# Optimization experiments

Hardware: AMD Instinct MI355X
Metric: run time of the kernel (lower is better)

Reference implementation:

```python
import jax, jax.numpy as jnp
import numpy as np

B, N, IN_DIM, D, H = 8, 1024, 128, 32, 8  # batch, nodes, in_dim, out_dim(per head), heads


def setup_inputs() -> dict:
    key = jax.random.key(0)
    ks = jax.random.split(key, 10)
    s = 1.0 / np.sqrt(IN_DIM)
    return {
        "h": jax.random.normal(ks[0], (B, N, IN_DIM), jnp.float32),
        "A": jax.random.randint(ks[1], (B, N, N), 0, 6, jnp.int32),  # hop distances
        "lengths": jax.random.randint(ks[2], (B,), 1, N + 1, jnp.int32),
        "alpha": jax.random.uniform(ks[3], (1,), jnp.float32, 0.1, 0.9),
        "Wq": jax.random.normal(ks[4], (H * D, IN_DIM), jnp.float32) * s,
        "bq": jax.random.normal(ks[5], (H * D,), jnp.float32) * 0.01,
        "Wk": jax.random.normal(ks[6], (H * D, IN_DIM), jnp.float32) * s,
        "bk": jax.random.normal(ks[7], (H * D,), jnp.float32) * 0.01,
        "Wv": jax.random.normal(ks[8], (H * D, IN_DIM), jnp.float32) * s,
        "bv": jax.random.normal(ks[9], (H * D,), jnp.float32) * 0.01,
    }


def reference(h, A, lengths, alpha, Wq, bq, Wk, bk, Wv, bv):
    b, n, _ = h.shape

    def proj(W, bvec):
        # [b, n, H*D] -> [b, H, n, D]
        return (h @ W.T + bvec).reshape(b, n, H, D).transpose(0, 2, 1, 3)

    Q, K, V = proj(Wq, bq), proj(Wk, bk), proj(Wv, bv)

    att = jnp.einsum("bhnd,bhmd->bhnm", Q, K)  # [b, H, n, n]
    pad = jnp.arange(n)[None, :] >= lengths[:, None]  # [b, n], True = padded node
    att = jnp.where(pad[:, None, None, :], -jnp.inf, att)  # mask key axis
    att = jax.nn.softmax(att / jnp.sqrt(jnp.asarray(D, att.dtype)), axis=-1)
    att = jnp.where(pad[:, None, :, None], jnp.asarray(0, att.dtype), att)  # zero padded query rows

    m1 = (A == 1)
    m2 = (A > 1)

    def masked_mean(a, m):
        mf = m[:, None, :, :].astype(a.dtype)
        cnt = H * jnp.sum(m)
        return jnp.sum(a * mf) / cnt.astype(a.dtype)

    pre_d1 = masked_mean(att, m1)
    pre_d2 = masked_mean(att, m2)

    # phi: adjacency-aware reweighting, att * alpha**A (hop-distance decay)
    att = att * jnp.power(alpha[0], A.astype(att.dtype))[:, None, :, :]

    post_d1 = masked_mean(att, m1)
    post_d2 = masked_mean(att, m2)

    h_heads = jnp.einsum("bhnm,bhmd->bhnd", att, V)  # [b, H, n, D]
    return h_heads, pre_d1, pre_d2, post_d1, post_d2
```

## Files before the change

kernel.cpp:

```cpp
#include <hip/hip_runtime.h>
#include <math.h>

#define BB 8
#define NN 1024
#define IND 128
#define DD 32
#define HH 8
#define KT 64
#define QT 64


__global__ __launch_bounds__(256) void proj_kernel(
    const float* __restrict__ h,
    const float* __restrict__ Wq, const float* __restrict__ bq,
    const float* __restrict__ Wk, const float* __restrict__ bk,
    const float* __restrict__ Wv, const float* __restrict__ bv,
    const int* __restrict__ lengths,
    float* __restrict__ Q, float* __restrict__ K, float* __restrict__ V)
{
    const int cb = blockIdx.x;
    const int rb = blockIdx.y;
    if (((rb & 15) * 64) >= lengths[rb >> 4]) return;

    const int t  = threadIdx.x;
    __shared__ float Xs[64][IND + 1];
    __shared__ float Ws[64][IND + 1];

    const int which = cb >> 2;
    const int c0    = (cb & 3) * 64;
    const float* Wsrc = (which == 0) ? Wq : (which == 1) ? Wk : Wv;
    const float* bsrc = (which == 0) ? bq : (which == 1) ? bk : bv;
    float* Out        = (which == 0) ? Q  : (which == 1) ? K  : V;

    #pragma unroll
    for (int i = 0; i < 8; ++i) {
        int e = (i * 256 + t) * 4;
        int r = e >> 7;
        int c = e & 127;
        float4 x = *(const float4*)(&h[(size_t)(rb * 64 + r) * IND + c]);
        Xs[r][c] = x.x; Xs[r][c + 1] = x.y; Xs[r][c + 2] = x.z; Xs[r][c + 3] = x.w;
        float4 w = *(const float4*)(&Wsrc[(size_t)(c0 + r) * IND + c]);
        Ws[r][c] = w.x; Ws[r][c + 1] = w.y; Ws[r][c + 2] = w.z; Ws[r][c + 3] = w.w;
    }
    __syncthreads();

    const int tr = (t >> 4) * 4;
    const int tc = (t & 15) * 4;
    float acc[4][4] = {};
    #pragma unroll 4
    for (int k = 0; k < IND; ++k) {
        float a0 = Xs[tr + 0][k], a1 = Xs[tr + 1][k], a2 = Xs[tr + 2][k], a3 = Xs[tr + 3][k];
        float w0 = Ws[tc + 0][k], w1 = Ws[tc + 1][k], w2 = Ws[tc + 2][k], w3 = Ws[tc + 3][k];
        acc[0][0] = fmaf(a0, w0, acc[0][0]); acc[0][1] = fmaf(a0, w1, acc[0][1]);
        acc[0][2] = fmaf(a0, w2, acc[0][2]); acc[0][3] = fmaf(a0, w3, acc[0][3]);
        acc[1][0] = fmaf(a1, w0, acc[1][0]); acc[1][1] = fmaf(a1, w1, acc[1][1]);
        acc[1][2] = fmaf(a1, w2, acc[1][2]); acc[1][3] = fmaf(a1, w3, acc[1][3]);
        acc[2][0] = fmaf(a2, w0, acc[2][0]); acc[2][1] = fmaf(a2, w1, acc[2][1]);
        acc[2][2] = fmaf(a2, w2, acc[2][2]); acc[2][3] = fmaf(a2, w3, acc[2][3]);
        acc[3][0] = fmaf(a3, w0, acc[3][0]); acc[3][1] = fmaf(a3, w1, acc[3][1]);
        acc[3][2] = fmaf(a3, w2, acc[3][2]); acc[3][3] = fmaf(a3, w3, acc[3][3]);
    }

    #pragma unroll
    for (int i = 0; i < 4; ++i) {
        int r = rb * 64 + tr + i;
        int bb = r >> 10, n = r & 1023;
        #pragma unroll
        for (int j = 0; j < 4; ++j) {
            int o = tc + j + c0;
            int hh = o >> 5, dd = o & 31;
            Out[(((size_t)bb * HH + hh) * NN + n) * DD + dd] = acc[i][j] + bsrc[o];
        }
    }
}

__global__ __launch_bounds__(256) void pack_kernel(
    const int* __restrict__ A, unsigned char* __restrict__ A8,
    unsigned long long* __restrict__ cnt)
{
    const int NT = (BB * NN * NN) / 4;
    unsigned c1 = 0, c2 = 0;
    for (int idx = blockIdx.x * 256 + threadIdx.x; idx < NT; idx += gridDim.x * 256) {
        int4 a = *(const int4*)&A[(size_t)idx * 4];
        unsigned packed = (unsigned)(a.x & 0xff) | ((unsigned)(a.y & 0xff) << 8) |
                          ((unsigned)(a.z & 0xff) << 16) | ((unsigned)(a.w & 0xff) << 24);
        *(unsigned*)&A8[(size_t)idx * 4] = packed;
        c1 += (a.x == 1) + (a.y == 1) + (a.z == 1) + (a.w == 1);
        c2 += (a.x > 1) + (a.y > 1) + (a.z > 1) + (a.w > 1);
    }
    #pragma unroll
    for (int off = 32; off; off >>= 1) {
        c1 += __shfl_down(c1, off);
        c2 += __shfl_down(c2, off);
    }
    __shared__ unsigned r1[4], r2[4];
    const int wave = threadIdx.x >> 6;
    if ((threadIdx.x & 63) == 0) { r1[wave] = c1; r2[wave] = c2; }
    __syncthreads();
    if (threadIdx.x == 0) {
        unsigned long long t1 = (unsigned long long)r1[0] + r1[1] + r1[2] + r1[3];
        unsigned long long t2 = (unsigned long long)r2[0] + r2[1] + r2[2] + r2[3];
        atomicAdd(&cnt[0], t1);
        atomicAdd(&cnt[32], t2);
    }
}

__global__ __launch_bounds__(256) void attn_kernel(
    const float* __restrict__ Q, const float* __restrict__ Kg, const float* __restrict__ Vg,
    const unsigned char* __restrict__ A8,
    const int* __restrict__ lengths, const float* __restrict__ alpha,
    float* __restrict__ out, double* __restrict__ sums)
{
    const int bid = blockIdx.x;
    const int qt = bid & 15;
    const int hh = (bid >> 4) & 7;
    const int b  = bid >> 7;
    const int t  = threadIdx.x;
    const int qg = t >> 3;
    const int lane8 = t & 7;

    const int len = lengths[b];
    const size_t base = ((size_t)b * HH + hh) * NN * DD;
    const int gq0 = qt * QT + qg;
    const int gq1 = gq0 + 32;

    if (qt * QT >= len) {
        float4 z = make_float4(0.f, 0.f, 0.f, 0.f);
        *(float4*)&out[base + (size_t)gq0 * DD + lane8 * 4] = z;
        *(float4*)&out[base + (size_t)gq1 * DD + lane8 * 4] = z;
        return;
    }

    __shared__ float Qs[QT][36];
    __shared__ float Ks[KT][36];
    __shared__ float Vs[KT][36];
    __shared__ unsigned char As[QT][80];
    __shared__ float red4[4][4];

    const float al  = alpha[0];
    const float l2a = __log2f(al);
    const float scale = 0.17677669529663687f;

    const int sr = t >> 3;
    const int sc = ((t & 7) - sr) & 7;

    #pragma unroll
    for (int i = 0; i < 2; ++i) {
        int r = i * 32 + sr;
        float4 v = *(const float4*)&Q[base + (size_t)(qt * QT + r) * DD + sc * 4];
        v.x *= scale; v.y *= scale; v.z *= scale; v.w *= scale;
        *(float4*)&Qs[r][sc * 4] = v;
    }

    float m0 = -1e30f, m1 = -1e30f, l0 = 0.f, l1 = 0.f;
    float acc0[32], acc1[32];
    #pragma unroll
    for (int d = 0; d < 32; ++d) { acc0[d] = 0.f; acc1[d] = 0.f; }
    float pr0_1 = 0.f, pr0_2 = 0.f, po0_1 = 0.f, po0_2 = 0.f;
    float pr1_1 = 0.f, pr1_2 = 0.f, po1_1 = 0.f, po1_2 = 0.f;

    for (int j0 = 0; j0 < len; j0 += KT) {
        __syncthreads();
        #pragma unroll
        for (int i = 0; i < 2; ++i) {
            int r = i * 32 + sr;
            *(float4*)&Ks[r][sc * 4] = *(const float4*)&Kg[base + (size_t)(j0 + r) * DD + sc * 4];
            *(float4*)&Vs[r][sc * 4] = *(const float4*)&Vg[base + (size_t)(j0 + r) * DD + sc * 4];
        }
        {
            int r = t >> 2, c = (t & 3) * 16;
            *(int4*)&As[r][c] = *(const int4*)&A8[((size_t)b * NN + qt * QT + r) * NN + j0 + c];
        }
        __syncthreads();

        float s0[8], s1[8];
        #pragma unroll
        for (int e = 0; e < 8; ++e) { s0[e] = 0.f; s1[e] = 0.f; }
        #pragma unroll
        for (int i = 0; i < 8; ++i) {
            float4 qa = *(const float4*)&Qs[qg][i * 4];
            float4 qb = *(const float4*)&Qs[qg + 32][i * 4];
            #pragma unroll
            for (int e = 0; e < 8; ++e) {
                float4 kv = *(const float4*)&Ks[e * 8 + lane8][i * 4];
                s0[e] = fmaf(qa.x, kv.x, s0[e]); s0[e] = fmaf(qa.y, kv.y, s0[e]);
                s0[e] = fmaf(qa.z, kv.z, s0[e]); s0[e] = fmaf(qa.w, kv.w, s0[e]);
                s1[e] = fmaf(qb.x, kv.x, s1[e]); s1[e] = fmaf(qb.y, kv.y, s1[e]);
                s1[e] = fmaf(qb.z, kv.z, s1[e]); s1[e] = fmaf(qb.w, kv.w, s1[e]);
            }
        }

        float tm0 = -INFINITY, tm1 = -INFINITY;
        #pragma unroll
        for (int e = 0; e < 8; ++e) {
            bool valid = (j0 + e * 8 + lane8) < len;
            s0[e] = valid ? s0[e] : -INFINITY;
            s1[e] = valid ? s1[e] : -INFINITY;
            tm0 = fmaxf(tm0, s0[e]); tm1 = fmaxf(tm1, s1[e]);
        }
        #pragma unroll
        for (int off = 1; off < 8; off <<= 1) {
            tm0 = fmaxf(tm0, __shfl_xor(tm0, off, 8));
            tm1 = fmaxf(tm1, __shfl_xor(tm1, off, 8));
        }
        if (tm0 > m0) {
            float scl = __expf(m0 - tm0);
            l0 *= scl; pr0_1 *= scl; pr0_2 *= scl; po0_1 *= scl; po0_2 *= scl;
            #pragma unroll
            for (int d = 0; d < 32; ++d) acc0[d] *= scl;
            m0 = tm0;
        }
        if (tm1 > m1) {
            float scl = __expf(m1 - tm1);
            l1 *= scl; pr1_1 *= scl; pr1_2 *= scl; po1_1 *= scl; po1_2 *= scl;
            #pragma unroll
            for (int d = 0; d < 32; ++d) acc1[d] *= scl;
            m1 = tm1;
        }

        #pragma unroll
        for (int e = 0; e < 8; ++e) {
            int j = e * 8 + lane8;
            float pe0 = __expf(s0[e] - m0);
            float pe1 = __expf(s1[e] - m1);
            l0 += pe0; l1 += pe1;
            int a0 = As[qg][j], a1 = As[qg + 32][j];
            float w0 = exp2f((float)a0 * l2a);
            float w1 = exp2f((float)a1 * l2a);
            float pw0 = pe0 * w0, pw1 = pe1 * w1;
            pr0_1 += (a0 == 1) ? pe0 : 0.f;  pr0_2 += (a0 > 1) ? pe0 : 0.f;
            po0_1 += (a0 == 1) ? pw0 : 0.f;  po0_2 += (a0 > 1) ? pw0 : 0.f;
            pr1_1 += (a1 == 1) ? pe1 : 0.f;  pr1_2 += (a1 > 1) ? pe1 : 0.f;
            po1_1 += (a1 == 1) ? pw1 : 0.f;  po1_2 += (a1 > 1) ? pw1 : 0.f;
            s0[e] = pw0; s1[e] = pw1;
        }

        #pragma unroll
        for (int e = 0; e < 8; ++e) {
            float pw0 = s0[e], pw1 = s1[e];
            #pragma unroll
            for (int i = 0; i < 8; ++i) {
                float4 vv = *(const float4*)&Vs[e * 8 + lane8][i * 4];
                acc0[i * 4 + 0] = fmaf(pw0, vv.x, acc0[i * 4 + 0]);
                acc0[i * 4 + 1] = fmaf(pw0, vv.y, acc0[i * 4 + 1]);
                acc0[i * 4 + 2] = fmaf(pw0, vv.z, acc0[i * 4 + 2]);
                acc0[i * 4 + 3] = fmaf(pw0, vv.w, acc0[i * 4 + 3]);
                acc1[i * 4 + 0] = fmaf(pw1, vv.x, acc1[i * 4 + 0]);
                acc1[i * 4 + 1] = fmaf(pw1, vv.y, acc1[i * 4 + 1]);
                acc1[i * 4 + 2] = fmaf(pw1, vv.z, acc1[i * 4 + 2]);
                acc1[i * 4 + 3] = fmaf(pw1, vv.w, acc1[i * 4 + 3]);
            }
        }
    }

    #pragma unroll
    for (int off = 1; off < 8; off <<= 1) {
        l0 += __shfl_xor(l0, off, 8);
        l1 += __shfl_xor(l1, off, 8);
    }
    const float inv0 = (gq0 < len) ? 1.f / l0 : 0.f;
    const float inv1 = (gq1 < len) ? 1.f / l1 : 0.f;

    #pragma unroll
    for (int off = 1; off < 8; off <<= 1) {
        #pragma unroll
        for (int d = 0; d < 32; ++d) {
            acc0[d] += __shfl_xor(acc0[d], off, 8);
            acc1[d] += __shfl_xor(acc1[d], off, 8);
        }
    }
    if (lane8 == 0) {
        #pragma unroll
        for (int i = 0; i < 8; ++i) {
            *(float4*)&out[base + (size_t)gq0 * DD + i * 4] =
                make_float4(acc0[i * 4 + 0] * inv0, acc0[i * 4 + 1] * inv0,
                            acc0[i * 4 + 2] * inv0, acc0[i * 4 + 3] * inv0);
            *(float4*)&out[base + (size_t)gq1 * DD + i * 4] =
                make_float4(acc1[i * 4 + 0] * inv1, acc1[i * 4 + 1] * inv1,
                            acc1[i * 4 + 2] * inv1, acc1[i * 4 + 3] * inv1);
        }
    }

    float v1 = pr0_1 * inv0 + pr1_1 * inv1;
    float v2 = pr0_2 * inv0 + pr1_2 * inv1;
    float v3 = po0_1 * inv0 + po1_1 * inv1;
    float v4 = po0_2 * inv0 + po1_2 * inv1;
    #pragma unroll
    for (int off = 1; off < 64; off <<= 1) {
        v1 += __shfl_xor(v1, off);
        v2 += __shfl_xor(v2, off);
        v3 += __shfl_xor(v3, off);
        v4 += __shfl_xor(v4, off);
    }
    const int wv = t >> 6;
    if ((t & 63) == 0) { red4[0][wv] = v1; red4[1][wv] = v2; red4[2][wv] = v3; red4[3][wv] = v4; }
    __syncthreads();
    if (t < 4) {
        float s = red4[t][0] + red4[t][1] + red4[t][2] + red4[t][3];
        atomicAdd(&sums[t * 32], (double)s);
    }
}

__global__ void fin_kernel(const double* __restrict__ sums,
                           const unsigned long long* __restrict__ cnt,
                           float* __restrict__ outtail)
{
    if (threadIdx.x == 0) {
        double c1 = (double)(cnt[0] * (unsigned long long)HH);
        double c2 = (double)(cnt[32] * (unsigned long long)HH);
        outtail[0] = (float)(sums[0]  / c1);
        outtail[1] = (float)(sums[32] / c2);
        outtail[2] = (float)(sums[64] / c1);
        outtail[3] = (float)(sums[96] / c2);
    }
}

extern "C" void kernel_launch(void* const* d_in, const int* in_sizes, int n_in,
                              void* d_out, int out_size, void* d_ws, size_t ws_size,
                              hipStream_t stream)
{
    const float* h   = (const float*)d_in[0];
    const int* A     = (const int*)d_in[1];
    const int* lens  = (const int*)d_in[2];
    const float* alp = (const float*)d_in[3];
    const float* Wq  = (const float*)d_in[4];
    const float* bq  = (const float*)d_in[5];
    const float* Wk  = (const float*)d_in[6];
    const float* bk  = (const float*)d_in[7];
    const float* Wv  = (const float*)d_in[8];
    const float* bv  = (const float*)d_in[9];

    float* outF = (float*)d_out;

    const size_t qkv = (size_t)BB * HH * NN * DD;
    float* Qw = (float*)d_ws;
    float* Kw = Qw + qkv;
    float* Vw = Kw + qkv;
    unsigned char* A8 = (unsigned char*)(Vw + qkv);
    double* sums = (double*)(A8 + (size_t)BB * NN * NN);
    unsigned long long* cnt = (unsigned long long*)(sums + 128);

    (void)hipMemsetAsync(sums, 0, 128 * sizeof(double) + 64 * sizeof(unsigned long long), stream);

    proj_kernel<<<dim3(12, 128), 256, 0, stream>>>(h, Wq, bq, Wk, bk, Wv, bv, lens, Qw, Kw, Vw);
    pack_kernel<<<1024, 256, 0, stream>>>(A, A8, cnt);
    attn_kernel<<<BB * HH * (NN / QT), 256, 0, stream>>>(Qw, Kw, Vw, A8, lens, alp, outF, sums);
    fin_kernel<<<1, 64, 0, stream>>>(sums, cnt, outF + qkv);
}
```

Before: 257.7 us.

## Split key tiles across two thread halves per block and merge softmax states

Attention blocks now use 512 threads where each 256-thread half processes alternating key tiles with its own K/V/A shared buffers. After the loop the halves merge their online-softmax max, sum, accumulators and masked-mean partials through shared memory. This shortens the serial key loop per block to reduce latency and load imbalance from long sequences, at the cost of more LDS per block, a merge step, and possible register pressure under the larger launch bound.

```diff
diff --git a/kernel.cpp b/kernel.cpp
--- a/kernel.cpp
+++ b/kernel.cpp
@@ -105,7 +105,7 @@
     }
 }
 
-__global__ __launch_bounds__(256) void attn_kernel(
+__global__ __launch_bounds__(512) void attn_kernel(
     const float* __restrict__ Q, const float* __restrict__ Kg, const float* __restrict__ Vg,
     const unsigned char* __restrict__ A8,
     const int* __restrict__ lengths, const float* __restrict__ alpha,
@@ -116,8 +116,10 @@
     const int hh = (bid >> 4) & 7;
     const int b  = bid >> 7;
     const int t  = threadIdx.x;
-    const int qg = t >> 3;
-    const int lane8 = t & 7;
+    const int half = t >> 8;
+    const int t2 = t & 255;
+    const int qg = t2 >> 3;
+    const int lane8 = t2 & 7;
 
     const int len = lengths[b];
     const size_t base = ((size_t)b * HH + hh) * NN * DD;
@@ -125,31 +127,37 @@
     const int gq1 = gq0 + 32;
 
     if (qt * QT >= len) {
-        float4 z = make_float4(0.f, 0.f, 0.f, 0.f);
-        *(float4*)&out[base + (size_t)gq0 * DD + lane8 * 4] = z;
-        *(float4*)&out[base + (size_t)gq1 * DD + lane8 * 4] = z;
+        if (t < 256) {
+            float4 z = make_float4(0.f, 0.f, 0.f, 0.f);
+            *(float4*)&out[base + (size_t)gq0 * DD + lane8 * 4] = z;
+            *(float4*)&out[base + (size_t)gq1 * DD + lane8 * 4] = z;
+        }
         return;
     }
 
-    __shared__ float Qs[QT][36];
-    __shared__ float Ks[KT][36];
-    __shared__ float Vs[KT][36];
-    __shared__ unsigned char As[QT][80];
-    __shared__ float red4[4][4];
+    __shared__ __align__(16) char smem[56448];
+    float (*Qs)[36]          = (float (*)[36])smem;
+    float (*Ks)[36]          = (float (*)[36])(smem + 9216 + half * 9216);
+    float (*Vs)[36]          = (float (*)[36])(smem + 27648 + half * 9216);
+    unsigned char (*Asl)[80] = (unsigned char (*)[80])(smem + 46080 + half * 5120);
+    float* mrg  = (float*)(smem + 46080);
+    float* redp = (float*)(smem + 56320);
 
     const float al  = alpha[0];
     const float l2a = __log2f(al);
     const float scale = 0.17677669529663687f;
 
-    const int sr = t >> 3;
-    const int sc = ((t & 7) - sr) & 7;
-
-    #pragma unroll
-    for (int i = 0; i < 2; ++i) {
-        int r = i * 32 + sr;
-        float4 v = *(const float4*)&Q[base + (size_t)(qt * QT + r) * DD + sc * 4];
-        v.x *= scale; v.y *= scale; v.z *= scale; v.w *= scale;
-        *(float4*)&Qs[r][sc * 4] = v;
+    const int sr = t2 >> 3;
+    const int sc = ((t2 & 7) - sr) & 7;
+
+    if (t < 256) {
+        #pragma unroll
+        for (int i = 0; i < 2; ++i) {
+            int r = i * 32 + sr;
+            float4 v = *(const float4*)&Q[base + (size_t)(qt * QT + r) * DD + sc * 4];
+            v.x *= scale; v.y *= scale; v.z *= scale; v.w *= scale;
+            *(float4*)&Qs[r][sc * 4] = v;
+        }
     }
 
     float m0 = -1e30f, m1 = -1e30f, l0 = 0.f, l1 = 0.f;
@@ -159,17 +167,22 @@
     float pr0_1 = 0.f, pr0_2 = 0.f, po0_1 = 0.f, po0_2 = 0.f;
     float pr1_1 = 0.f, pr1_2 = 0.f, po1_1 = 0.f, po1_2 = 0.f;
 
-    for (int j0 = 0; j0 < len; j0 += KT) {
+    const int ntiles = (len + KT - 1) / KT;
+    const int nit = (ntiles + 1) >> 1;
+
+    for (int it = 0; it < nit; ++it) {
+        const int j0  = (2 * it + half) * KT;
+        const int j0c = (j0 < len) ? j0 : 0;
         __syncthreads();
         #pragma unroll
         for (int i = 0; i < 2; ++i) {
             int r = i * 32 + sr;
-            *(float4*)&Ks[r][sc * 4] = *(const float4*)&Kg[base + (size_t)(j0 + r) * DD + sc * 4];
-            *(float4*)&Vs[r][sc * 4] = *(const float4*)&Vg[base + (size_t)(j0 + r) * DD + sc * 4];
+            *(float4*)&Ks[r][sc * 4] = *(const float4*)&Kg[base + (size_t)(j0c + r) * DD + sc * 4];
+            *(float4*)&Vs[r][sc * 4] = *(const float4*)&Vg[base + (size_t)(j0c + r) * DD + sc * 4];
         }
         {
-            int r = t >> 2, c = (t & 3) * 16;
-            *(int4*)&As[r][c] = *(const int4*)&A8[((size_t)b * NN + qt * QT + r) * NN + j0 + c];
+            int r = t2 >> 2, c = (t2 & 3) * 16;
+            *(int4*)&Asl[r][c] = *(const int4*)&A8[((size_t)b * NN + qt * QT + r) * NN + j0c + c];
         }
         __syncthreads();
 
@@ -224,7 +237,7 @@
             float pe0 = __expf(s0[e] - m0);
             float pe1 = __expf(s1[e] - m1);
             l0 += pe0; l1 += pe1;
-            int a0 = As[qg][j], a1 = As[qg + 32][j];
+            int a0 = Asl[qg][j], a1 = Asl[qg + 32][j];
             float w0 = exp2f((float)a0 * l2a);
             float w1 = exp2f((float)a1 * l2a);
             float pw0 = pe0 * w0, pw1 = pe1 * w1;
@@ -255,36 +268,76 @@
 
     #pragma unroll
     for (int off = 1; off < 8; off <<= 1) {
-        l0 += __shfl_xor(l0, off, 8);
-        l1 += __shfl_xor(l1, off, 8);
-    }
-    const float inv0 = (gq0 < len) ? 1.f / l0 : 0.f;
-    const float inv1 = (gq1 < len) ? 1.f / l1 : 0.f;
-
-    #pragma unroll
-    for (int off = 1; off < 8; off <<= 1) {
+        l0 += __shfl_xor(l0, off, 8);       l1 += __shfl_xor(l1, off, 8);
+        pr0_1 += __shfl_xor(pr0_1, off, 8); pr0_2 += __shfl_xor(pr0_2, off, 8);
+        po0_1 += __shfl_xor(po0_1, off, 8); po0_2 += __shfl_xor(po0_2, off, 8);
+        pr1_1 += __shfl_xor(pr1_1, off, 8); pr1_2 += __shfl_xor(pr1_2, off, 8);
+        po1_1 += __shfl_xor(po1_1, off, 8); po1_2 += __shfl_xor(po1_2, off, 8);
         #pragma unroll
         for (int d = 0; d < 32; ++d) {
             acc0[d] += __shfl_xor(acc0[d], off, 8);
             acc1[d] += __shfl_xor(acc1[d], off, 8);
         }
     }
-    if (lane8 == 0) {
-        #pragma unroll
-        for (int i = 0; i < 8; ++i) {
-            *(float4*)&out[base + (size_t)gq0 * DD + i * 4] =
-                make_float4(acc0[i * 4 + 0] * inv0, acc0[i * 4 + 1] * inv0,
-                            acc0[i * 4 + 2] * inv0, acc0[i * 4 + 3] * inv0);
-            *(float4*)&out[base + (size_t)gq1 * DD + i * 4] =
-                make_float4(acc1[i * 4 + 0] * inv1, acc1[i * 4 + 1] * inv1,
-                            acc1[i * 4 + 2] * inv1, acc1[i * 4 + 3] * inv1);
-        }
-    }
-
-    float v1 = pr0_1 * inv0 + pr1_1 * inv1;
-    float v2 = pr0_2 * inv0 + pr1_2 * inv1;
-    float v3 = po0_1 * inv0 + po1_1 * inv1;
-    float v4 = po0_2 * inv0 + po1_2 * inv1;
+
+    __syncthreads();
+    if (half == 1 && lane8 == 0) {
+        float* r = &mrg[(size_t)qg * 40];
+        r[0] = m0; r[1] = l0; r[2] = pr0_1; r[3] = pr0_2; r[4] = po0_1; r[5] = po0_2;
+        #pragma unroll
+        for (int d = 0; d < 32; ++d) r[6 + d] = acc0[d];
+        float* r2 = &mrg[(size_t)(qg + 32) * 40];
+        r2[0] = m1; r2[1] = l1; r2[2] = pr1_1; r2[3] = pr1_2; r2[4] = po1_1; r2[5] = po1_2;
+        #pragma unroll
+        for (int d = 0; d < 32; ++d) r2[6 + d] = acc1[d];
+    }
+    __syncthreads();
+
+    float v1 = 0.f, v2 = 0.f, v3 = 0.f, v4 = 0.f;
+    if (half == 0) {
+        const int dsl = lane8 * 4;
+        {
+            const float* r = &mrg[(size_t)qg * 40];
+            float mB = r[0], LB = r[1];
+            float ms = fmaxf(m0, mB);
+            float fA = __expf(m0 - ms), fB = __expf(mB - ms);
+            float L = l0 * fA + LB * fB;
+            float inv = (gq0 < len) ? 1.f / L : 0.f;
+            float4 o;
+            o.x = (acc0[dsl + 0] * fA + r[6 + dsl + 0] * fB) * inv;
+            o.y = (acc0[dsl + 1] * fA + r[6 + dsl + 1] * fB) * inv;
+            o.z = (acc0[dsl + 2] * fA + r[6 + dsl + 2] * fB) * inv;
+            o.w = (acc0[dsl + 3] * fA + r[6 + dsl + 3] * fB) * inv;
+            *(float4*)&out[base + (size_t)gq0 * DD + dsl] = o;
+            if (lane8 == 0) {
+                v1 += (pr0_1 * fA + r[2] * fB) * inv;
+                v2 += (pr0_2 * fA + r[3] * fB) * inv;
+                v3 += (po0_1 * fA + r[4] * fB) * inv;
+                v4 += (po0_2 * fA + r[5] * fB) * inv;
+            }
+        }
+        {
+            const float* r = &mrg[(size_t)(qg + 32) * 40];
+            float mB = r[0], LB = r[1];
+            float ms = fmaxf(m1, mB);
+            float fA = __expf(m1 - ms), fB = __expf(mB - ms);
+            float L = l1 * fA + LB * fB;
+            float inv = (gq1 < len) ? 1.f / L : 0.f;
+            float4 o;
+            o.x = (acc1[dsl + 0] * fA + r[6 + dsl + 0] * fB) * inv;
+            o.y = (acc1[dsl + 1] * fA + r[6 + dsl + 1] * fB) * inv;
+            o.z = (acc1[dsl + 2] * fA + r[6 + dsl + 2] * fB) * inv;
+            o.w = (acc1[dsl + 3] * fA + r[6 + dsl + 3] * fB) * inv;
+            *(float4*)&out[base + (size_t)gq1 * DD + dsl] = o;
+            if (lane8 == 0) {
+                v1 += (pr1_1 * fA + r[2] * fB) * inv;
+                v2 += (pr1_2 * fA + r[3] * fB) * inv;
+                v3 += (po1_1 * fA + r[4] * fB) * inv;
+                v4 += (po1_2 * fA + r[5] * fB) * inv;
+            }
+        }
+    }
+
     #pragma unroll
     for (int off = 1; off < 64; off <<= 1) {
         v1 += __shfl_xor(v1, off);
@@ -293,10 +346,16 @@
         v4 += __shfl_xor(v4, off);
     }
     const int wv = t >> 6;
-    if ((t & 63) == 0) { red4[0][wv] = v1; red4[1][wv] = v2; red4[2][wv] = v3; red4[3][wv] = v4; }
+    __syncthreads();
+    if ((t & 63) == 0) {
+        redp[0 * 8 + wv] = v1; redp[1 * 8 + wv] = v2;
+        redp[2 * 8 + wv] = v3; redp[3 * 8 + wv] = v4;
+    }
     __syncthreads();
     if (t < 4) {
-        float s = red4[t][0] + red4[t][1] + red4[t][2] + red4[t][3];
+        float s = 0.f;
+        #pragma unroll
+        for (int w = 0; w < 8; ++w) s += redp[t * 8 + w];
         atomicAdd(&sums[t * 32], (double)s);
     }
 }
@@ -344,6 +403,6 @@
 
     proj_kernel<<<dim3(12, 128), 256, 0, stream>>>(h, Wq, bq, Wk, bk, Wv, bv, lens, Qw, Kw, Vw);
     pack_kernel<<<1024, 256, 0, stream>>>(A, A8, cnt);
-    attn_kernel<<<BB * HH * (NN / QT), 256, 0, stream>>>(Qw, Kw, Vw, A8, lens, alp, outF, sums);
+    attn_kernel<<<BB * HH * (NN / QT), 512, 0, stream>>>(Qw, Kw, Vw, A8, lens, alp, outF, sums);
     fin_kernel<<<1, 64, 0, stream>>>(sums, cnt, outF + qkv);
 }
```

Measured after the change: 623.5 us. 142% more time.

## Split attention key range in two blocks and merge partial softmax results

Applied to the files above, without the earlier changes.

Adds a split-K flash-attention variant in which each query tile is processed by two blocks, each covering half of the key tiles. Partial max, denominator, mask statistics and accumulators go to a workspace buffer, and a separate merge kernel rescales and combines them, writes the output and accumulates the masked means. This doubles the grid to improve occupancy and load balance when sequence lengths vary. The cost is an extra kernel launch plus partial-result traffic, and the new path only runs when the workspace is large enough.

```diff
diff --git a/kernel.cpp b/kernel.cpp
--- a/kernel.cpp
+++ b/kernel.cpp
@@ -105,6 +105,7 @@
     }
 }
 
+
 __global__ __launch_bounds__(256) void attn_kernel(
     const float* __restrict__ Q, const float* __restrict__ Kg, const float* __restrict__ Vg,
     const unsigned char* __restrict__ A8,
@@ -301,6 +302,246 @@
     }
 }
 
+__global__ __launch_bounds__(256) void attn_split_kernel(
+    const float* __restrict__ Q, const float* __restrict__ Kg, const float* __restrict__ Vg,
+    const unsigned char* __restrict__ A8,
+    const int* __restrict__ lengths, const float* __restrict__ alpha,
+    float* __restrict__ part)
+{
+    const int bidAll = blockIdx.x;
+    const int split = bidAll >> 10;
+    const int bid = bidAll & 1023;
+    const int qt = bid & 15;
+    const int hh = (bid >> 4) & 7;
+    const int b  = bid >> 7;
+    const int t  = threadIdx.x;
+    const int qg = t >> 3;
+    const int lane8 = t & 7;
+
+    const int len = lengths[b];
+    const size_t base = ((size_t)b * HH + hh) * NN * DD;
+
+    if (qt * QT >= len) return;
+
+    __shared__ float Qs[QT][36];
+    __shared__ float Ks[KT][36];
+    __shared__ float Vs[KT][36];
+    __shared__ unsigned char As[QT][80];
+
+    const float al  = alpha[0];
+    const float l2a = __log2f(al);
+    const float scale = 0.17677669529663687f;
+
+    const int sr = t >> 3;
+    const int sc = ((t & 7) - sr) & 7;
+
+    #pragma unroll
+    for (int i = 0; i < 2; ++i) {
+        int r = i * 32 + sr;
+        float4 v = *(const float4*)&Q[base + (size_t)(qt * QT + r) * DD + sc * 4];
+        v.x *= scale; v.y *= scale; v.z *= scale; v.w *= scale;
+        *(float4*)&Qs[r][sc * 4] = v;
+    }
+
+    float m0 = -1e30f, m1 = -1e30f, l0 = 0.f, l1 = 0.f;
+    float acc0[32], acc1[32];
+    #pragma unroll
+    for (int d = 0; d < 32; ++d) { acc0[d] = 0.f; acc1[d] = 0.f; }
+    float pr0_1 = 0.f, pr0_2 = 0.f, po0_1 = 0.f, po0_2 = 0.f;
+    float pr1_1 = 0.f, pr1_2 = 0.f, po1_1 = 0.f, po1_2 = 0.f;
+
+    const int ntiles = (len + KT - 1) / KT;
+    const int htiles = (ntiles + 1) >> 1;
+    const int t0 = split * htiles;
+    const int t1 = (ntiles < t0 + htiles) ? ntiles : (t0 + htiles);
+
+    for (int tt = t0; tt < t1; ++tt) {
+        const int j0 = tt * KT;
+        __syncthreads();
+        #pragma unroll
+        for (int i = 0; i < 2; ++i) {
+            int r = i * 32 + sr;
+            *(float4*)&Ks[r][sc * 4] = *(const float4*)&Kg[base + (size_t)(j0 + r) * DD + sc * 4];
+            *(float4*)&Vs[r][sc * 4] = *(const float4*)&Vg[base + (size_t)(j0 + r) * DD + sc * 4];
+        }
+        {
+            int r = t >> 2, c = (t & 3) * 16;
+            *(int4*)&As[r][c] = *(const int4*)&A8[((size_t)b * NN + qt * QT + r) * NN + j0 + c];
+        }
+        __syncthreads();
+
+        float s0[8], s1[8];
+        #pragma unroll
+        for (int e = 0; e < 8; ++e) { s0[e] = 0.f; s1[e] = 0.f; }
+        #pragma unroll
+        for (int i = 0; i < 8; ++i) {
+            float4 qa = *(const float4*)&Qs[qg][i * 4];
+            float4 qb = *(const float4*)&Qs[qg + 32][i * 4];
+            #pragma unroll
+            for (int e = 0; e < 8; ++e) {
+                float4 kv = *(const float4*)&Ks[e * 8 + lane8][i * 4];
+                s0[e] = fmaf(qa.x, kv.x, s0[e]); s0[e] = fmaf(qa.y, kv.y, s0[e]);
+                s0[e] = fmaf(qa.z, kv.z, s0[e]); s0[e] = fmaf(qa.w, kv.w, s0[e]);
+                s1[e] = fmaf(qb.x, kv.x, s1[e]); s1[e] = fmaf(qb.y, kv.y, s1[e]);
+                s1[e] = fmaf(qb.z, kv.z, s1[e]); s1[e] = fmaf(qb.w, kv.w, s1[e]);
+            }
+        }
+
+        float tm0 = -INFINITY, tm1 = -INFINITY;
+        #pragma unroll
+        for (int e = 0; e < 8; ++e) {
+            bool valid = (j0 + e * 8 + lane8) < len;
+            s0[e] = valid ? s0[e] : -INFINITY;
+            s1[e] = valid ? s1[e] : -INFINITY;
+            tm0 = fmaxf(tm0, s0[e]); tm1 = fmaxf(tm1, s1[e]);
+        }
+        #pragma unroll
+        for (int off = 1; off < 8; off <<= 1) {
+            tm0 = fmaxf(tm0, __shfl_xor(tm0, off, 8));
+            tm1 = fmaxf(tm1, __shfl_xor(tm1, off, 8));
+        }
+        if (tm0 > m0) {
+            float scl = __expf(m0 - tm0);
+            l0 *= scl; pr0_1 *= scl; pr0_2 *= scl; po0_1 *= scl; po0_2 *= scl;
+            #pragma unroll
+            for (int d = 0; d < 32; ++d) acc0[d] *= scl;
+            m0 = tm0;
+        }
+        if (tm1 > m1) {
+            float scl = __expf(m1 - tm1);
+            l1 *= scl; pr1_1 *= scl; pr1_2 *= scl; po1_1 *= scl; po1_2 *= scl;
+            #pragma unroll
+            for (int d = 0; d < 32; ++d) acc1[d] *= scl;
+            m1 = tm1;
+        }
+
+        #pragma unroll
+        for (int e = 0; e < 8; ++e) {
+            int j = e * 8 + lane8;
+            float pe0 = __expf(s0[e] - m0);
+            float pe1 = __expf(s1[e] - m1);
+            l0 += pe0; l1 += pe1;
+            int a0 = As[qg][j], a1 = As[qg + 32][j];
+            float w0 = exp2f((float)a0 * l2a);
+            float w1 = exp2f((float)a1 * l2a);
+            float pw0 = pe0 * w0, pw1 = pe1 * w1;
+            pr0_1 += (a0 == 1) ? pe0 : 0.f;  pr0_2 += (a0 > 1) ? pe0 : 0.f;
+            po0_1 += (a0 == 1) ? pw0 : 0.f;  po0_2 += (a0 > 1) ? pw0 : 0.f;
+            pr1_1 += (a1 == 1) ? pe1 : 0.f;  pr1_2 += (a1 > 1) ? pe1 : 0.f;
+            po1_1 += (a1 == 1) ? pw1 : 0.f;  po1_2 += (a1 > 1) ? pw1 : 0.f;
+            s0[e] = pw0; s1[e] = pw1;
+        }
+
+        #pragma unroll
+        for (int e = 0; e < 8; ++e) {
+            float pw0 = s0[e], pw1 = s1[e];
+            #pragma unroll
+            for (int i = 0; i < 8; ++i) {
+                float4 vv = *(const float4*)&Vs[e * 8 + lane8][i * 4];
+                acc0[i * 4 + 0] = fmaf(pw0, vv.x, acc0[i * 4 + 0]);
+                acc0[i * 4 + 1] = fmaf(pw0, vv.y, acc0[i * 4 + 1]);
+                acc0[i * 4 + 2] = fmaf(pw0, vv.z, acc0[i * 4 + 2]);
+                acc0[i * 4 + 3] = fmaf(pw0, vv.w, acc0[i * 4 + 3]);
+                acc1[i * 4 + 0] = fmaf(pw1, vv.x, acc1[i * 4 + 0]);
+                acc1[i * 4 + 1] = fmaf(pw1, vv.y, acc1[i * 4 + 1]);
+                acc1[i * 4 + 2] = fmaf(pw1, vv.z, acc1[i * 4 + 2]);
+                acc1[i * 4 + 3] = fmaf(pw1, vv.w, acc1[i * 4 + 3]);
+            }
+        }
+    }
+
+    #pragma unroll
+    for (int off = 1; off < 8; off <<= 1) {
+        l0 += __shfl_xor(l0, off, 8);       l1 += __shfl_xor(l1, off, 8);
+        pr0_1 += __shfl_xor(pr0_1, off, 8); pr0_2 += __shfl_xor(pr0_2, off, 8);
+        po0_1 += __shfl_xor(po0_1, off, 8); po0_2 += __shfl_xor(po0_2, off, 8);
+        pr1_1 += __shfl_xor(pr1_1, off, 8); pr1_2 += __shfl_xor(pr1_2, off, 8);
+        po1_1 += __shfl_xor(po1_1, off, 8); po1_2 += __shfl_xor(po1_2, off, 8);
+        #pragma unroll
+        for (int d = 0; d < 32; ++d) {
+            acc0[d] += __shfl_xor(acc0[d], off, 8);
+            acc1[d] += __shfl_xor(acc1[d], off, 8);
+        }
+    }
+
+    const int dsl = lane8 * 4;
+    float* st0 = part + (((size_t)split * 1024 + bid) * 64 + qg) * 40;
+    float* st1 = st0 + 32 * 40;
+    if (lane8 == 0) {
+        st0[0] = m0; st0[1] = l0; st0[2] = pr0_1; st0[3] = pr0_2; st0[4] = po0_1; st0[5] = po0_2;
+        st1[0] = m1; st1[1] = l1; st1[2] = pr1_1; st1[3] = pr1_2; st1[4] = po1_1; st1[5] = po1_2;
+    }
+    *(float4*)&st0[8 + dsl] = make_float4(acc0[dsl], acc0[dsl + 1], acc0[dsl + 2], acc0[dsl + 3]);
+    *(float4*)&st1[8 + dsl] = make_float4(acc1[dsl], acc1[dsl + 1], acc1[dsl + 2], acc1[dsl + 3]);
+}
+
+__global__ __launch_bounds__(256) void merge_kernel(
+    const float* __restrict__ part, const int* __restrict__ lengths,
+    float* __restrict__ out, double* __restrict__ sums)
+{
+    const int bid = blockIdx.x;
+    const int qt = bid & 15;
+    const int hh = (bid >> 4) & 7;
+    const int b  = bid >> 7;
+    const int t  = threadIdx.x;
+    const int qg = t >> 3;
+    const int lane8 = t & 7;
+    const int dsl = lane8 * 4;
+    const int len = lengths[b];
+    const size_t base = ((size_t)b * HH + hh) * NN * DD;
+
+    if (qt * QT >= len) {
+        float4 z = make_float4(0.f, 0.f, 0.f, 0.f);
+        *(float4*)&out[base + (size_t)(qt * QT + qg) * DD + dsl] = z;
+        *(float4*)&out[base + (size_t)(qt * QT + qg + 32) * DD + dsl] = z;
+        return;
+    }
+
+    float v1 = 0.f, v2 = 0.f, v3 = 0.f, v4 = 0.f;
+    #pragma unroll
+    for (int rr = 0; rr < 2; ++rr) {
+        const int row = qg + rr * 32;
+        const int gq = qt * QT + row;
+        const float* sA = part + (((size_t)0 * 1024 + bid) * 64 + row) * 40;
+        const float* sB = part + (((size_t)1 * 1024 + bid) * 64 + row) * 40;
+        float mA = sA[0], lA = sA[1], mB = sB[0], lB = sB[1];
+        float ms = fmaxf(mA, mB);
+        float fA = __expf(mA - ms), fB = __expf(mB - ms);
+        float L = lA * fA + lB * fB;
+        float inv = (gq < len) ? 1.f / L : 0.f;
+        float4 aA = *(const float4*)&sA[8 + dsl];
+        float4 aB = *(const float4*)&sB[8 + dsl];
+        float4 o;
+        o.x = (aA.x * fA + aB.x * fB) * inv;
+        o.y = (aA.y * fA + aB.y * fB) * inv;
+        o.z = (aA.z * fA + aB.z * fB) * inv;
+        o.w = (aA.w * fA + aB.w * fB) * inv;
+        *(float4*)&out[base + (size_t)gq * DD + dsl] = o;
+        if (lane8 == 0) {
+            v1 += (sA[2] * fA + sB[2] * fB) * inv;
+            v2 += (sA[3] * fA + sB[3] * fB) * inv;
+            v3 += (sA[4] * fA + sB[4] * fB) * inv;
+            v4 += (sA[5] * fA + sB[5] * fB) * inv;
+        }
+    }
+
+    __shared__ float red4[4][4];
+    #pragma unroll
+    for (int off = 1; off < 64; off <<= 1) {
+        v1 += __shfl_xor(v1, off);
+        v2 += __shfl_xor(v2, off);
+        v3 += __shfl_xor(v3, off);
+        v4 += __shfl_xor(v4, off);
+    }
+    const int wv = t >> 6;
+    if ((t & 63) == 0) { red4[0][wv] = v1; red4[1][wv] = v2; red4[2][wv] = v3; red4[3][wv] = v4; }
+    __syncthreads();
+    if (t < 4) {
+        float s = red4[t][0] + red4[t][1] + red4[t][2] + red4[t][3];
+        atomicAdd(&sums[t * 32], (double)s);
+    }
+}
+
 __global__ void fin_kernel(const double* __restrict__ sums,
                            const unsigned long long* __restrict__ cnt,
                            float* __restrict__ outtail)
@@ -339,11 +580,19 @@
     unsigned char* A8 = (unsigned char*)(Vw + qkv);
     double* sums = (double*)(A8 + (size_t)BB * NN * NN);
     unsigned long long* cnt = (unsigned long long*)(sums + 128);
+    float* part = (float*)(cnt + 64);
+
+    const size_t need = (size_t)((char*)(part + (size_t)2048 * 64 * 40) - (char*)d_ws);
 
     (void)hipMemsetAsync(sums, 0, 128 * sizeof(double) + 64 * sizeof(unsigned long long), stream);
 
     proj_kernel<<<dim3(12, 128), 256, 0, stream>>>(h, Wq, bq, Wk, bk, Wv, bv, lens, Qw, Kw, Vw);
     pack_kernel<<<1024, 256, 0, stream>>>(A, A8, cnt);
-    attn_kernel<<<BB * HH * (NN / QT), 256, 0, stream>>>(Qw, Kw, Vw, A8, lens, alp, outF, sums);
+    if (ws_size >= need) {
+        attn_split_kernel<<<2048, 256, 0, stream>>>(Qw, Kw, Vw, A8, lens, alp, part);
+        merge_kernel<<<1024, 256, 0, stream>>>(part, lens, outF, sums);
+    } else {
+        attn_kernel<<<1024, 256, 0, stream>>>(Qw, Kw, Vw, A8, lens, alp, outF, sums);
+    }
     fin_kernel<<<1, 64, 0, stream>>>(sums, cnt, outF + qkv);
 }
```

Result: no change. 255.4 us (-0.9%).

## Split attention key range across two blocks, merge partial softmax states, vectorize projection

Applied to the files above, without the earlier changes.

The attention kernel now splits each query tile's key tiles between two blocks. Each block writes its partial max, sum, masked-mean statistics and accumulators to a workspace, and a new merge kernel combines them with log-sum-exp rescaling. The aim is more parallelism and better load balance across variable-length batches, at the cost of an extra launch and extra global memory traffic for the partial states. The projection kernel also switches to float4 shared-memory loads with a strided thread-to-output mapping, and the pack kernel grid is doubled.

```diff
diff --git a/kernel.cpp b/kernel.cpp
--- a/kernel.cpp
+++ b/kernel.cpp
@@ -23,8 +23,8 @@
     if (((rb & 15) * 64) >= lengths[rb >> 4]) return;
 
     const int t  = threadIdx.x;
-    __shared__ float Xs[64][IND + 1];
-    __shared__ float Ws[64][IND + 1];
+    __shared__ float Xs[64][132];
+    __shared__ float Ws[64][132];
 
     const int which = cb >> 2;
     const int c0    = (cb & 3) * 64;
@@ -37,37 +37,39 @@
         int e = (i * 256 + t) * 4;
         int r = e >> 7;
         int c = e & 127;
-        float4 x = *(const float4*)(&h[(size_t)(rb * 64 + r) * IND + c]);
-        Xs[r][c] = x.x; Xs[r][c + 1] = x.y; Xs[r][c + 2] = x.z; Xs[r][c + 3] = x.w;
-        float4 w = *(const float4*)(&Wsrc[(size_t)(c0 + r) * IND + c]);
-        Ws[r][c] = w.x; Ws[r][c + 1] = w.y; Ws[r][c + 2] = w.z; Ws[r][c + 3] = w.w;
+        *(float4*)&Xs[r][c] = *(const float4*)(&h[(size_t)(rb * 64 + r) * IND + c]);
+        *(float4*)&Ws[r][c] = *(const float4*)(&Wsrc[(size_t)(c0 + r) * IND + c]);
     }
     __syncthreads();
 
-    const int tr = (t >> 4) * 4;
-    const int tc = (t & 15) * 4;
+    const int tr = t >> 4;
+    const int tc = t & 15;
     float acc[4][4] = {};
-    #pragma unroll 4
-    for (int k = 0; k < IND; ++k) {
-        float a0 = Xs[tr + 0][k], a1 = Xs[tr + 1][k], a2 = Xs[tr + 2][k], a3 = Xs[tr + 3][k];
-        float w0 = Ws[tc + 0][k], w1 = Ws[tc + 1][k], w2 = Ws[tc + 2][k], w3 = Ws[tc + 3][k];
-        acc[0][0] = fmaf(a0, w0, acc[0][0]); acc[0][1] = fmaf(a0, w1, acc[0][1]);
-        acc[0][2] = fmaf(a0, w2, acc[0][2]); acc[0][3] = fmaf(a0, w3, acc[0][3]);
-        acc[1][0] = fmaf(a1, w0, acc[1][0]); acc[1][1] = fmaf(a1, w1, acc[1][1]);
-        acc[1][2] = fmaf(a1, w2, acc[1][2]); acc[1][3] = fmaf(a1, w3, acc[1][3]);
-        acc[2][0] = fmaf(a2, w0, acc[2][0]); acc[2][1] = fmaf(a2, w1, acc[2][1]);
-        acc[2][2] = fmaf(a2, w2, acc[2][2]); acc[2][3] = fmaf(a2, w3, acc[2][3]);
-        acc[3][0] = fmaf(a3, w0, acc[3][0]); acc[3][1] = fmaf(a3, w1, acc[3][1]);
-        acc[3][2] = fmaf(a3, w2, acc[3][2]); acc[3][3] = fmaf(a3, w3, acc[3][3]);
+    for (int k = 0; k < IND; k += 4) {
+        float4 xa[4], wb[4];
+        #pragma unroll
+        for (int i = 0; i < 4; ++i) xa[i] = *(const float4*)&Xs[tr + i * 16][k];
+        #pragma unroll
+        for (int j = 0; j < 4; ++j) wb[j] = *(const float4*)&Ws[tc + j * 16][k];
+        #pragma unroll
+        for (int i = 0; i < 4; ++i) {
+            #pragma unroll
+            for (int j = 0; j < 4; ++j) {
+                acc[i][j] = fmaf(xa[i].x, wb[j].x, acc[i][j]);
+                acc[i][j] = fmaf(xa[i].y, wb[j].y, acc[i][j]);
+                acc[i][j] = fmaf(xa[i].z, wb[j].z, acc[i][j]);
+                acc[i][j] = fmaf(xa[i].w, wb[j].w, acc[i][j]);
+            }
+        }
     }
 
     #pragma unroll
     for (int i = 0; i < 4; ++i) {
-        int r = rb * 64 + tr + i;
+        int r = rb * 64 + tr + i * 16;
         int bb = r >> 10, n = r & 1023;
         #pragma unroll
         for (int j = 0; j < 4; ++j) {
-            int o = tc + j + c0;
+            int o = tc + j * 16 + c0;
             int hh = o >> 5, dd = o & 31;
             Out[(((size_t)bb * HH + hh) * NN + n) * DD + dd] = acc[i][j] + bsrc[o];
         }
@@ -105,13 +107,15 @@
     }
 }
 
-__global__ __launch_bounds__(256) void attn_kernel(
+__global__ __launch_bounds__(256) void attn_split_kernel(
     const float* __restrict__ Q, const float* __restrict__ Kg, const float* __restrict__ Vg,
     const unsigned char* __restrict__ A8,
     const int* __restrict__ lengths, const float* __restrict__ alpha,
-    float* __restrict__ out, double* __restrict__ sums)
-{
-    const int bid = blockIdx.x;
+    float* __restrict__ part)
+{
+    const int bidAll = blockIdx.x;
+    const int split = bidAll >> 10;
+    const int bid = bidAll & 1023;
     const int qt = bid & 15;
     const int hh = (bid >> 4) & 7;
     const int b  = bid >> 7;
@@ -121,21 +125,13 @@
 
     const int len = lengths[b];
     const size_t base = ((size_t)b * HH + hh) * NN * DD;
-    const int gq0 = qt * QT + qg;
-    const int gq1 = gq0 + 32;
-
-    if (qt * QT >= len) {
-        float4 z = make_float4(0.f, 0.f, 0.f, 0.f);
-        *(float4*)&out[base + (size_t)gq0 * DD + lane8 * 4] = z;
-        *(float4*)&out[base + (size_t)gq1 * DD + lane8 * 4] = z;
-        return;
-    }
+
+    if (qt * QT >= len) return;
 
     __shared__ float Qs[QT][36];
     __shared__ float Ks[KT][36];
     __shared__ float Vs[KT][36];
     __shared__ unsigned char As[QT][80];
-    __shared__ float red4[4][4];
 
     const float al  = alpha[0];
     const float l2a = __log2f(al);
@@ -159,7 +155,13 @@
     float pr0_1 = 0.f, pr0_2 = 0.f, po0_1 = 0.f, po0_2 = 0.f;
     float pr1_1 = 0.f, pr1_2 = 0.f, po1_1 = 0.f, po1_2 = 0.f;
 
-    for (int j0 = 0; j0 < len; j0 += KT) {
+    const int ntiles = (len + KT - 1) / KT;
+    const int htiles = (ntiles + 1) >> 1;
+    const int t0 = split * htiles;
+    const int t1 = (ntiles < t0 + htiles) ? ntiles : (t0 + htiles);
+
+    for (int tt = t0; tt < t1; ++tt) {
+        const int j0 = tt * KT;
         __syncthreads();
         #pragma unroll
         for (int i = 0; i < 2; ++i) {
@@ -255,36 +257,80 @@
 
     #pragma unroll
     for (int off = 1; off < 8; off <<= 1) {
-        l0 += __shfl_xor(l0, off, 8);
-        l1 += __shfl_xor(l1, off, 8);
-    }
-    const float inv0 = (gq0 < len) ? 1.f / l0 : 0.f;
-    const float inv1 = (gq1 < len) ? 1.f / l1 : 0.f;
-
-    #pragma unroll
-    for (int off = 1; off < 8; off <<= 1) {
+        l0 += __shfl_xor(l0, off, 8);       l1 += __shfl_xor(l1, off, 8);
+        pr0_1 += __shfl_xor(pr0_1, off, 8); pr0_2 += __shfl_xor(pr0_2, off, 8);
+        po0_1 += __shfl_xor(po0_1, off, 8); po0_2 += __shfl_xor(po0_2, off, 8);
+        pr1_1 += __shfl_xor(pr1_1, off, 8); pr1_2 += __shfl_xor(pr1_2, off, 8);
+        po1_1 += __shfl_xor(po1_1, off, 8); po1_2 += __shfl_xor(po1_2, off, 8);
         #pragma unroll
         for (int d = 0; d < 32; ++d) {
             acc0[d] += __shfl_xor(acc0[d], off, 8);
             acc1[d] += __shfl_xor(acc1[d], off, 8);
         }
     }
+
+    const int dsl = lane8 * 4;
+    float* st0 = part + (((size_t)split * 1024 + bid) * 64 + qg) * 40;
+    float* st1 = st0 + 32 * 40;
     if (lane8 == 0) {
-        #pragma unroll
-        for (int i = 0; i < 8; ++i) {
-            *(float4*)&out[base + (size_t)gq0 * DD + i * 4] =
-                make_float4(acc0[i * 4 + 0] * inv0, acc0[i * 4 + 1] * inv0,
-                            acc0[i * 4 + 2] * inv0, acc0[i * 4 + 3] * inv0);
-            *(float4*)&out[base + (size_t)gq1 * DD + i * 4] =
-                make_float4(acc1[i * 4 + 0] * inv1, acc1[i * 4 + 1] * inv1,
-                            acc1[i * 4 + 2] * inv1, acc1[i * 4 + 3] * inv1);
-        }
-    }
-
-    float v1 = pr0_1 * inv0 + pr1_1 * inv1;
-    float v2 = pr0_2 * inv0 + pr1_2 * inv1;
-    float v3 = po0_1 * inv0 + po1_1 * inv1;
-    float v4 = po0_2 * inv0 + po1_2 * inv1;
+        st0[0] = m0; st0[1] = l0; st0[2] = pr0_1; st0[3] = pr0_2; st0[4] = po0_1; st0[5] = po0_2;
+        st1[0] = m1; st1[1] = l1; st1[2] = pr1_1; st1[3] = pr1_2; st1[4] = po1_1; st1[5] = po1_2;
+    }
+    *(float4*)&st0[8 + dsl] = make_float4(acc0[dsl], acc0[dsl + 1], acc0[dsl + 2], acc0[dsl + 3]);
+    *(float4*)&st1[8 + dsl] = make_float4(acc1[dsl], acc1[dsl + 1], acc1[dsl + 2], acc1[dsl + 3]);
+}
+
+__global__ __launch_bounds__(256) void merge_kernel(
+    const float* __restrict__ part, const int* __restrict__ lengths,
+    float* __restrict__ out, double* __restrict__ sums)
+{
+    const int bid = blockIdx.x;
+    const int qt = bid & 15;
+    const int hh = (bid >> 4) & 7;
+    const int b  = bid >> 7;
+    const int t  = threadIdx.x;
+    const int qg = t >> 3;
+    const int lane8 = t & 7;
+    const int dsl = lane8 * 4;
+    const int len = lengths[b];
+    const size_t base = ((size_t)b * HH + hh) * NN * DD;
+
+    if (qt * QT >= len) {
+        float4 z = make_float4(0.f, 0.f, 0.f, 0.f);
+        *(float4*)&out[base + (size_t)(qt * QT + qg) * DD + dsl] = z;
+        *(float4*)&out[base + (size_t)(qt * QT + qg + 32) * DD + dsl] = z;
+        return;
+    }
+
+    float v1 = 0.f, v2 = 0.f, v3 = 0.f, v4 = 0.f;
+    #pragma unroll
+    for (int rr = 0; rr < 2; ++rr) {
+        const int row = qg + rr * 32;
+        const int gq = qt * QT + row;
+        const float* sA = part + (((size_t)0 * 1024 + bid) * 64 + row) * 40;
+        const float* sB = part + (((size_t)1 * 1024 + bid) * 64 + row) * 40;
+        float mA = sA[0], lA = sA[1], mB = sB[0], lB = sB[1];
+        float ms = fmaxf(mA, mB);
+        float fA = __expf(mA - ms), fB = __expf(mB - ms);
+        float L = lA * fA + lB * fB;
+        float inv = (gq < len) ? 1.f / L : 0.f;
+        float4 aA = *(const float4*)&sA[8 + dsl];
+        float4 aB = *(const float4*)&sB[8 + dsl];
+        float4 o;
+        o.x = (aA.x * fA + aB.x * fB) * inv;
+        o.y = (aA.y * fA + aB.y * fB) * inv;
+        o.z = (aA.z * fA + aB.z * fB) * inv;
+        o.w = (aA.w * fA + aB.w * fB) * inv;
+        *(float4*)&out[base + (size_t)gq * DD + dsl] = o;
+        if (lane8 == 0) {
+            v1 += (sA[2] * fA + sB[2] * fB) * inv;
+            v2 += (sA[3] * fA + sB[3] * fB) * inv;
+            v3 += (sA[4] * fA + sB[4] * fB) * inv;
+            v4 += (sA[5] * fA + sB[5] * fB) * inv;
+        }
+    }
+
+    __shared__ float red4[4][4];
     #pragma unroll
     for (int off = 1; off < 64; off <<= 1) {
         v1 += __shfl_xor(v1, off);
@@ -339,11 +385,13 @@
     unsigned char* A8 = (unsigned char*)(Vw + qkv);
     double* sums = (double*)(A8 + (size_t)BB * NN * NN);
     unsigned long long* cnt = (unsigned long long*)(sums + 128);
+    float* part = (float*)(cnt + 64);
 
     (void)hipMemsetAsync(sums, 0, 128 * sizeof(double) + 64 * sizeof(unsigned long long), stream);
 
     proj_kernel<<<dim3(12, 128), 256, 0, stream>>>(h, Wq, bq, Wk, bk, Wv, bv, lens, Qw, Kw, Vw);
-    pack_kernel<<<1024, 256, 0, stream>>>(A, A8, cnt);
-    attn_kernel<<<BB * HH * (NN / QT), 256, 0, stream>>>(Qw, Kw, Vw, A8, lens, alp, outF, sums);
+    pack_kernel<<<2048, 256, 0, stream>>>(A, A8, cnt);
+    attn_split_kernel<<<2048, 256, 0, stream>>>(Qw, Kw, Vw, A8, lens, alp, part);
+    merge_kernel<<<1024, 256, 0, stream>>>(part, lens, outF, sums);
     fin_kernel<<<1, 64, 0, stream>>>(sums, cnt, outF + qkv);
 }
```

Result: no change. 257.0 us (-0.3%).
